# Kernel optimization log

Hardware: AMD Instinct MI355X
Metric: run time of the kernel (lower is better)

## Reference

```python
import jax, jax.numpy as jnp
import numpy as np
from functools import partial

HIDDEN = 512
INTER = 2048
N_EXPERTS = 8
TOP_K = 2
BATCH, SEQ = 2, 2048


def setup_inputs() -> dict:
    key = jax.random.key(0)
    k_x, k_r, k_u, k_d = jax.random.split(key, 4)
    x = jax.random.normal(k_x, (BATCH, SEQ, HIDDEN), dtype=jnp.float32)
    # router: nn.Linear(hidden, n_experts, bias=False); store as (H, E) so logits = x @ w_router
    w_router = jax.random.normal(k_r, (HIDDEN, N_EXPERTS), dtype=jnp.float32) / np.sqrt(HIDDEN)
    # per-expert FFN weights, stored pre-transposed for x @ W
    w_up = jax.random.normal(k_u, (N_EXPERTS, HIDDEN, INTER), dtype=jnp.float32) / np.sqrt(HIDDEN)
    w_down = jax.random.normal(k_d, (N_EXPERTS, INTER, HIDDEN), dtype=jnp.float32) / np.sqrt(INTER)
    return {"x": x, "w_router": w_router, "w_up": w_up, "w_down": w_down}


def _moe_forward(x, w_router, w_up, w_down):
    B, S, H = x.shape
    T = B * S
    xf = x.reshape(T, H)
    logits = xf @ w_router                      # (T, E)
    top_vals, top_idx = jax.lax.top_k(logits, TOP_K)
    rw = jax.nn.softmax(top_vals, axis=-1)      # (T, K) routing weights
    E = w_up.shape[0]
    # combine weight per (token, expert): sum_k rw[t,k] * [sel[t,k]==e]
    cw = jnp.zeros((T, E), dtype=x.dtype).at[
        jnp.arange(T)[:, None], top_idx
    ].add(rw)                                   # (T, E)

    def expert_step(acc, operand):
        wu, wd, we = operand                    # (H,I), (I,H), (T,)
        h = jax.nn.gelu(xf @ wu, approximate=False)  # exact erf GELU (torch nn.GELU default)
        y = h @ wd                              # (T, H)
        return acc + we[:, None] * y, None

    acc0 = jnp.zeros((T, H), dtype=x.dtype)
    acc, _ = jax.lax.scan(expert_step, acc0, (w_up, w_down, cw.T))
    output = acc.reshape(B, S, H)

    # aux load-balance loss
    probs = jax.nn.softmax(logits, axis=-1)
    expert_usage = probs.mean(axis=0)           # (E,)
    load_balance_loss = jnp.sum((expert_usage - 1.0 / E) ** 2)
    return output, load_balance_loss, expert_usage


def reference(x, w_router, w_up, w_down):
    return _moe_forward(x, w_router, w_up, w_down)
```

## Files before the change

kernel.cpp:

```cpp
#include <hip/hip_runtime.h>
#include <hip/hip_bf16.h>
#include <math.h>

#define T_TOKENS 4096
#define HID 512
#define INTER 2048
#define NEXP 8

typedef __bf16 bf16x8 __attribute__((ext_vector_type(8)));
typedef __bf16 bf16x4 __attribute__((ext_vector_type(4)));
typedef float f32x4 __attribute__((ext_vector_type(4)));

#define GLD16(g, l) __builtin_amdgcn_global_load_lds( \
    (const __attribute__((address_space(1))) void*)(g), \
    (__attribute__((address_space(3))) void*)(l), 16, 0, 0)

__device__ __forceinline__ void transpose_tile(const float* __restrict__ in,
                                               __bf16* __restrict__ out,
                                               int R, int C, int r0, int c0,
                                               __bf16 (*tile)[68]) {
  int tid = threadIdx.x;
  int rr = tid >> 4;
  int cc = (tid & 15) * 4;
#pragma unroll
  for (int j = 0; j < 4; ++j) {
    int row = j * 16 + rr;
    float4 v = *(const float4*)(in + (size_t)(r0 + row) * C + c0 + cc);
    tile[row][cc + 0] = (__bf16)v.x;
    tile[row][cc + 1] = (__bf16)v.y;
    tile[row][cc + 2] = (__bf16)v.z;
    tile[row][cc + 3] = (__bf16)v.w;
  }
  __syncthreads();
#pragma unroll
  for (int j = 0; j < 4; ++j) {
    int orow = j * 16 + rr;
    bf16x4 o;
    o[0] = tile[cc + 0][orow];
    o[1] = tile[cc + 1][orow];
    o[2] = tile[cc + 2][orow];
    o[3] = tile[cc + 3][orow];
    *(bf16x4*)(out + (size_t)(c0 + orow) * R + r0 + cc) = o;
  }
}

__global__ void prep_kernel(const float* __restrict__ x, const float* __restrict__ wrt,
                            int* __restrict__ topi, float* __restrict__ topw,
                            int* __restrict__ cntpart, float* __restrict__ usagepart,
                            const float* __restrict__ wu, __bf16* __restrict__ wuT,
                            const float* __restrict__ wd, __bf16* __restrict__ wdT) {
  __shared__ float wsm[8 * 512];
  __shared__ float us[8];
  __shared__ int cs[8];
  __shared__ __bf16 tile[64][68];
  int bid = blockIdx.x;
  int tid = threadIdx.x;

  if (bid >= 3072) {
    int b = bid - 3072;
    int e = b >> 8;
    int c0 = (b & 7) * 64;
    int r0 = ((b >> 3) & 31) * 64;
    transpose_tile(wd + (size_t)e * INTER * HID, wdT + (size_t)e * INTER * HID,
                   INTER, HID, r0, c0, tile);
    return;
  }
  if (bid >= 1024) {
    int b = bid - 1024;
    int e = b >> 8;
    int c0 = (b & 31) * 64;
    int r0 = ((b >> 5) & 7) * 64;
    transpose_tile(wu + (size_t)e * HID * INTER, wuT + (size_t)e * HID * INTER,
                   HID, INTER, r0, c0, tile);
    return;
  }

  if (tid < 8) { us[tid] = 0.f; cs[tid] = 0; }
  for (int i = tid; i < 8 * 512; i += 256) {
    int e = i >> 9, h = i & 511;
    wsm[i] = wrt[h * 8 + e];
  }
  __syncthreads();
  int lane = tid & 63;
  int t = bid * 4 + (tid >> 6);
  const float* xt = x + (size_t)t * HID;
  float a[8];
#pragma unroll
  for (int e = 0; e < 8; ++e) a[e] = 0.f;
#pragma unroll
  for (int j = 0; j < 8; ++j) {
    float xv = xt[lane + j * 64];
#pragma unroll
    for (int e = 0; e < 8; ++e) a[e] += xv * wsm[e * 512 + lane + j * 64];
  }
#pragma unroll
  for (int off = 32; off > 0; off >>= 1) {
#pragma unroll
    for (int e = 0; e < 8; ++e) a[e] += __shfl_xor(a[e], off);
  }
  if (lane == 0) {
    float m = a[0];
#pragma unroll
    for (int e = 1; e < 8; ++e) m = fmaxf(m, a[e]);
    float p[8], s = 0.f;
#pragma unroll
    for (int e = 0; e < 8; ++e) { p[e] = expf(a[e] - m); s += p[e]; }
    float inv = 1.f / s;
#pragma unroll
    for (int e = 0; e < 8; ++e) atomicAdd(&us[e], p[e] * inv);
    int i0 = 0; float v0 = a[0];
#pragma unroll
    for (int e = 1; e < 8; ++e) if (a[e] > v0) { v0 = a[e]; i0 = e; }
    int i1 = -1; float v1 = -3.4e38f;
#pragma unroll
    for (int e = 0; e < 8; ++e) if (e != i0 && a[e] > v1) { v1 = a[e]; i1 = e; }
    float e1 = expf(v1 - v0);
    float w0 = 1.f / (1.f + e1);
    float w1 = e1 * w0;
    topi[t * 2] = i0; topi[t * 2 + 1] = i1;
    topw[t * 2] = w0; topw[t * 2 + 1] = w1;
    atomicAdd(&cs[i0], 1); atomicAdd(&cs[i1], 1);
  }
  __syncthreads();
  if (tid < 8) {
    cntpart[bid * 8 + tid] = cs[tid];
    usagepart[bid * 8 + tid] = us[tid];
  }
}

__global__ void finalize_kernel(const int* __restrict__ cntpart, const float* __restrict__ usagepart,
                                int* __restrict__ cnt, int* __restrict__ off,
                                float* __restrict__ tail) {
  __shared__ int ci[256];
  __shared__ float uf[256];
  int tid = threadIdx.x;
  int e = tid >> 5, c = tid & 31;
  int s = 0; float u = 0.f;
  for (int b = c; b < 1024; b += 32) {
    s += cntpart[b * 8 + e];
    u += usagepart[b * 8 + e];
  }
  ci[tid] = s; uf[tid] = u;
  __syncthreads();
  for (int st = 16; st > 0; st >>= 1) {
    if (c < st) { ci[tid] += ci[tid + st]; uf[tid] += uf[tid + st]; }
    __syncthreads();
  }
  if (tid == 0) {
    int o = 0;
    float loss = 0.f;
    for (int e2 = 0; e2 < 8; ++e2) {
      int ce = ci[e2 * 32];
      cnt[e2] = ce;
      off[e2] = o;
      o += (ce + 127) & ~127;
      float uu = uf[e2 * 32] * (1.0f / 4096.0f);
      tail[1 + e2] = uu;
      float d = uu - 0.125f;
      loss += d * d;
    }
    tail[0] = loss;
  }
}

__global__ void slotassign_kernel(const int* __restrict__ topi, const float* __restrict__ topw,
                                  const int* __restrict__ off, int* __restrict__ cnt2pad,
                                  int* __restrict__ stok, float* __restrict__ sw,
                                  int* __restrict__ slotof) {
  __shared__ int wavehist[16][8];
  __shared__ int blockbase[8];
  int tid = threadIdx.x, lane = tid & 63, wv = tid >> 6;
  int p = blockIdx.x * 1024 + tid;
  int e = topi[p];
  float w = topw[p];
  unsigned long long mymask = 0;
#pragma unroll
  for (int e2 = 0; e2 < 8; ++e2) {
    unsigned long long m = __ballot(e == e2);
    if (lane == 0) wavehist[wv][e2] = __popcll(m);
    if (e2 == e) mymask = m;
  }
  __syncthreads();
  if (tid < 8) {
    int s = 0;
#pragma unroll
    for (int w2 = 0; w2 < 16; ++w2) s += wavehist[w2][tid];
    blockbase[tid] = atomicAdd(&cnt2pad[tid * 16], s);
  }
  __syncthreads();
  int rank = 0;
  for (int w2 = 0; w2 < wv; ++w2) rank += wavehist[w2][e];
  rank += __popcll(mymask & ((1ull << lane) - 1ull));
  int slot = off[e] + blockbase[e] + rank;
  stok[slot] = p >> 1;
  sw[slot] = w;
  slotof[p] = slot;
}

__global__ void gather_kernel(const float* __restrict__ x, const int* __restrict__ slotof,
                              __bf16* __restrict__ Xg) {
  int tid = threadIdx.x, lane = tid & 63;
  int p = blockIdx.x * 4 + (tid >> 6);
  int slot = slotof[p];
  int t = p >> 1;
  const float4* xs = (const float4*)(x + (size_t)t * HID);
  float4 v0 = xs[lane * 2], v1 = xs[lane * 2 + 1];
  bf16x8 o;
  o[0] = (__bf16)v0.x; o[1] = (__bf16)v0.y; o[2] = (__bf16)v0.z; o[3] = (__bf16)v0.w;
  o[4] = (__bf16)v1.x; o[5] = (__bf16)v1.y; o[6] = (__bf16)v1.z; o[7] = (__bf16)v1.w;
  *(bf16x8*)(Xg + (size_t)slot * HID + lane * 8) = o;
}

template <int EPI>
__launch_bounds__(256, 8)
__global__ void gemm64(const __bf16* __restrict__ A, const __bf16* __restrict__ Ball,
                       int lda, int ldb, long sB,
                       __bf16* __restrict__ Hout, int ldh,
                       float* __restrict__ Out,
                       const int* __restrict__ stok, const float* __restrict__ sw,
                       const int* __restrict__ offp, const int* __restrict__ cntp) {
  int bid = blockIdx.x;
  int e = bid & 7;
  int r = bid >> 3;
  int mt, n0, nk;
  if (EPI == 0) {
    n0 = (r & 31) * 64;
    mt = r >> 5;
    nk = 8;
  } else {
    n0 = (r & 7) * 64;
    mt = r >> 3;
    nk = 32;
  }
  int cnte = cntp[e];
  if (mt * 64 >= cnte) return;
  int offe = offp[e];
  int m0 = offe + mt * 64;
  const __bf16* B = Ball + (size_t)e * sB;

  __shared__ char smem[16384];
  char* As = smem;
  char* Bs = smem + 8192;

  int tid = threadIdx.x;
  int lane = tid & 63;
  int wid = tid >> 6;
  int wr = wid >> 1, wc = wid & 1;

  f32x4 acc[2][2];
#pragma unroll
  for (int i = 0; i < 2; ++i)
#pragma unroll
    for (int j = 0; j < 2; ++j) acc[i][j] = (f32x4){0.f, 0.f, 0.f, 0.f};

  for (int it = 0; it < nk; ++it) {
    int k0 = it * 64;
#pragma unroll
    for (int q2 = 0; q2 < 2; ++q2) {
      int L = q2 * 4096 + tid * 16;
      int row = L >> 7;
      int kb = L & 127;
      int kbs = kb ^ ((row & 7) << 4);
      GLD16((const char*)(A + (size_t)(m0 + row) * lda + k0) + kbs, As + L);
      GLD16((const char*)(B + (size_t)(n0 + row) * (size_t)ldb + k0) + kbs, Bs + L);
    }
    __syncthreads();
#pragma unroll
    for (int ks = 0; ks < 2; ++ks) {
      bf16x8 av[2], bv[2];
      int kb = ks * 64 + ((lane >> 4) << 4);
#pragma unroll
      for (int i = 0; i < 2; ++i) {
        int rowA = wr * 32 + i * 16 + (lane & 15);
        av[i] = *(const bf16x8*)(As + rowA * 128 + (kb ^ ((rowA & 7) << 4)));
        int rowB = wc * 32 + i * 16 + (lane & 15);
        bv[i] = *(const bf16x8*)(Bs + rowB * 128 + (kb ^ ((rowB & 7) << 4)));
      }
#pragma unroll
      for (int i = 0; i < 2; ++i)
#pragma unroll
        for (int j = 0; j < 2; ++j)
          acc[i][j] = __builtin_amdgcn_mfma_f32_16x16x32_bf16(av[i], bv[j], acc[i][j], 0, 0, 0);
    }
    __syncthreads();
  }

  int lim = offe + cnte;
  if (EPI == 0) {
#pragma unroll
    for (int i = 0; i < 2; ++i) {
#pragma unroll
      for (int r2 = 0; r2 < 4; ++r2) {
        int slot = m0 + wr * 32 + i * 16 + ((lane >> 4) << 2) + r2;
        if (slot < lim) {
          __bf16* hp = Hout + (size_t)slot * ldh + n0 + wc * 32 + (lane & 15);
#pragma unroll
          for (int j = 0; j < 2; ++j) {
            float v = acc[i][j][r2];
            float g = 0.5f * v * (1.0f + erff(v * 0.70710678118654752f));
            hp[j * 16] = (__bf16)g;
          }
        }
      }
    }
  } else {
#pragma unroll
    for (int i = 0; i < 2; ++i) {
#pragma unroll
      for (int r2 = 0; r2 < 4; ++r2) {
        int slot = m0 + wr * 32 + i * 16 + ((lane >> 4) << 2) + r2;
        if (slot < lim) {
          int t = stok[slot];
          float w = sw[slot];
          float* op = Out + (size_t)t * HID + n0 + wc * 32 + (lane & 15);
#pragma unroll
          for (int j = 0; j < 2; ++j) atomicAdd(op + j * 16, w * acc[i][j][r2]);
        }
      }
    }
  }
}

extern "C" void kernel_launch(void* const* d_in, const int* in_sizes, int n_in,
                              void* d_out, int out_size, void* d_ws, size_t ws_size,
                              hipStream_t stream) {
  const float* x   = (const float*)d_in[0];
  const float* wrt = (const float*)d_in[1];
  const float* wu  = (const float*)d_in[2];
  const float* wd  = (const float*)d_in[3];
  float* out = (float*)d_out;
  char* ws = (char*)d_ws;

  const size_t XG_OFF   = 0;
  const size_t H_OFF    = XG_OFF  + (size_t)9216 * 512 * 2;
  const size_t WUT_OFF  = H_OFF   + (size_t)9216 * 2048 * 2;
  const size_t WDT_OFF  = WUT_OFF + (size_t)8 * 512 * 2048 * 2;
  const size_t TOK_OFF  = WDT_OFF + (size_t)8 * 512 * 2048 * 2;
  const size_t SW_OFF   = TOK_OFF  + (size_t)9216 * 4;
  const size_t TOPI_OFF = SW_OFF   + (size_t)9216 * 4;
  const size_t TOPW_OFF = TOPI_OFF + (size_t)8192 * 4;
  const size_t SLOT_OFF = TOPW_OFF + (size_t)8192 * 4;
  const size_t CPART_OFF = SLOT_OFF + (size_t)8192 * 4;
  const size_t UPART_OFF = CPART_OFF + (size_t)8192 * 4;
  const size_t CTRL_OFF  = UPART_OFF + (size_t)8192 * 4;

  __bf16* Xg   = (__bf16*)(ws + XG_OFF);
  __bf16* H    = (__bf16*)(ws + H_OFF);
  __bf16* wuT  = (__bf16*)(ws + WUT_OFF);
  __bf16* wdT  = (__bf16*)(ws + WDT_OFF);
  int*    stok = (int*)(ws + TOK_OFF);
  float*  sw   = (float*)(ws + SW_OFF);
  int*    topi = (int*)(ws + TOPI_OFF);
  float*  topw = (float*)(ws + TOPW_OFF);
  int*    slotof = (int*)(ws + SLOT_OFF);
  int*    cntpart = (int*)(ws + CPART_OFF);
  float*  usagepart = (float*)(ws + UPART_OFF);
  int*    cnt  = (int*)(ws + CTRL_OFF);
  int*    off  = (int*)(ws + CTRL_OFF + 64);
  int*    cnt2pad = (int*)(ws + CTRL_OFF + 128);

  hipMemsetAsync(ws + CTRL_OFF, 0, 1024, stream);
  hipMemsetAsync(d_out, 0, (size_t)T_TOKENS * HID * 4, stream);

  prep_kernel<<<5120, 256, 0, stream>>>(x, wrt, topi, topw, cntpart, usagepart,
                                        wu, wuT, wd, wdT);
  finalize_kernel<<<1, 256, 0, stream>>>(cntpart, usagepart, cnt, off,
                                         out + (size_t)T_TOKENS * HID);
  slotassign_kernel<<<8, 1024, 0, stream>>>(topi, topw, off, cnt2pad, stok, sw, slotof);
  gather_kernel<<<2048, 256, 0, stream>>>(x, slotof, Xg);

  gemm64<0><<<6144, 256, 0, stream>>>(
      Xg, wuT, HID, HID, (long)INTER * HID, H, INTER,
      nullptr, nullptr, nullptr, off, cnt);
  gemm64<1><<<1536, 256, 0, stream>>>(
      H, wdT, INTER, INTER, (long)INTER * HID, nullptr, 0,
      out, stok, sw, off, cnt);
}
```

Baseline: 123.1 us.

## Fold slot assignment into finalize and gather, drop slotassign kernel and memset

The finalize kernel now computes per-block, per-expert base offsets with a prefix scan over the partial counts. Each gather wave then derives its token's two expert slots locally from topi and those bases, and writes the metadata itself. This removes the separate slotassign launch, its atomics, and a memset. Gather now reads each x row once and writes two bf16 rows, which halves the gather grid. The single-block finalize does slightly more serial work, and slot order becomes deterministic.

```diff
diff --git a/kernel.cpp b/kernel.cpp
--- a/kernel.cpp
+++ b/kernel.cpp
@@ -130,85 +130,87 @@
 
 __global__ void finalize_kernel(const int* __restrict__ cntpart, const float* __restrict__ usagepart,
                                 int* __restrict__ cnt, int* __restrict__ off,
-                                float* __restrict__ tail) {
-  __shared__ int ci[256];
-  __shared__ float uf[256];
+                                int* __restrict__ bbase, float* __restrict__ tail) {
+  __shared__ int cs[8][32];
+  __shared__ float uf[8][32];
+  __shared__ int cpre[8][32];
+  __shared__ int ctot[8];
+  __shared__ int offs[8];
   int tid = threadIdx.x;
   int e = tid >> 5, c = tid & 31;
   int s = 0; float u = 0.f;
-  for (int b = c; b < 1024; b += 32) {
+  for (int b = c * 32; b < c * 32 + 32; ++b) {
     s += cntpart[b * 8 + e];
     u += usagepart[b * 8 + e];
   }
-  ci[tid] = s; uf[tid] = u;
-  __syncthreads();
-  for (int st = 16; st > 0; st >>= 1) {
-    if (c < st) { ci[tid] += ci[tid + st]; uf[tid] += uf[tid + st]; }
-    __syncthreads();
-  }
+  cs[e][c] = s; uf[e][c] = u;
+  __syncthreads();
+  if (c == 0) {
+    int run = 0;
+#pragma unroll
+    for (int cc = 0; cc < 32; ++cc) { cpre[e][cc] = run; run += cs[e][cc]; }
+    ctot[e] = run;
+    cnt[e] = run;
+  }
+  __syncthreads();
   if (tid == 0) {
     int o = 0;
     float loss = 0.f;
     for (int e2 = 0; e2 < 8; ++e2) {
-      int ce = ci[e2 * 32];
-      cnt[e2] = ce;
+      offs[e2] = o;
       off[e2] = o;
-      o += (ce + 127) & ~127;
-      float uu = uf[e2 * 32] * (1.0f / 4096.0f);
+      o += (ctot[e2] + 127) & ~127;
+      float uu = 0.f;
+      for (int cc = 0; cc < 32; ++cc) uu += uf[e2][cc];
+      uu *= (1.0f / 4096.0f);
       tail[1 + e2] = uu;
       float d = uu - 0.125f;
       loss += d * d;
     }
     tail[0] = loss;
   }
-}
-
-__global__ void slotassign_kernel(const int* __restrict__ topi, const float* __restrict__ topw,
-                                  const int* __restrict__ off, int* __restrict__ cnt2pad,
-                                  int* __restrict__ stok, float* __restrict__ sw,
-                                  int* __restrict__ slotof) {
-  __shared__ int wavehist[16][8];
-  __shared__ int blockbase[8];
-  int tid = threadIdx.x, lane = tid & 63, wv = tid >> 6;
-  int p = blockIdx.x * 1024 + tid;
-  int e = topi[p];
-  float w = topw[p];
-  unsigned long long mymask = 0;
-#pragma unroll
-  for (int e2 = 0; e2 < 8; ++e2) {
-    unsigned long long m = __ballot(e == e2);
-    if (lane == 0) wavehist[wv][e2] = __popcll(m);
-    if (e2 == e) mymask = m;
-  }
-  __syncthreads();
-  if (tid < 8) {
-    int s = 0;
-#pragma unroll
-    for (int w2 = 0; w2 < 16; ++w2) s += wavehist[w2][tid];
-    blockbase[tid] = atomicAdd(&cnt2pad[tid * 16], s);
-  }
-  __syncthreads();
-  int rank = 0;
-  for (int w2 = 0; w2 < wv; ++w2) rank += wavehist[w2][e];
-  rank += __popcll(mymask & ((1ull << lane) - 1ull));
-  int slot = off[e] + blockbase[e] + rank;
-  stok[slot] = p >> 1;
-  sw[slot] = w;
-  slotof[p] = slot;
-}
-
-__global__ void gather_kernel(const float* __restrict__ x, const int* __restrict__ slotof,
+  __syncthreads();
+  int base = offs[e] + cpre[e][c];
+  for (int b = c * 32; b < c * 32 + 32; ++b) {
+    bbase[b * 8 + e] = base;
+    base += cntpart[b * 8 + e];
+  }
+}
+
+__global__ void gather_kernel(const float* __restrict__ x, const int* __restrict__ topi,
+                              const float* __restrict__ topw, const int* __restrict__ bbase,
+                              int* __restrict__ stok, float* __restrict__ sw,
                               __bf16* __restrict__ Xg) {
   int tid = threadIdx.x, lane = tid & 63;
-  int p = blockIdx.x * 4 + (tid >> 6);
-  int slot = slotof[p];
-  int t = p >> 1;
+  int t = blockIdx.x * 4 + (tid >> 6);
+  int b = t >> 2;
+  int j = t & 3;
+  int slot0 = 0, slot1 = 0;
+  if (lane == 0) {
+    int ti[8];
+#pragma unroll
+    for (int q = 0; q < 8; ++q) ti[q] = topi[b * 8 + q];
+    int e0 = ti[2 * j], e1 = ti[2 * j + 1];
+    int r0 = 0, r1 = 0;
+#pragma unroll
+    for (int q = 0; q < 8; ++q) {
+      if (q < 2 * j) { r0 += (ti[q] == e0); r1 += (ti[q] == e1); }
+    }
+    r1 += (e0 == e1);
+    slot0 = bbase[b * 8 + e0] + r0;
+    slot1 = bbase[b * 8 + e1] + r1;
+    stok[slot0] = t; sw[slot0] = topw[2 * t];
+    stok[slot1] = t; sw[slot1] = topw[2 * t + 1];
+  }
+  slot0 = __shfl(slot0, 0);
+  slot1 = __shfl(slot1, 0);
   const float4* xs = (const float4*)(x + (size_t)t * HID);
   float4 v0 = xs[lane * 2], v1 = xs[lane * 2 + 1];
   bf16x8 o;
   o[0] = (__bf16)v0.x; o[1] = (__bf16)v0.y; o[2] = (__bf16)v0.z; o[3] = (__bf16)v0.w;
   o[4] = (__bf16)v1.x; o[5] = (__bf16)v1.y; o[6] = (__bf16)v1.z; o[7] = (__bf16)v1.w;
-  *(bf16x8*)(Xg + (size_t)slot * HID + lane * 8) = o;
+  *(bf16x8*)(Xg + (size_t)slot0 * HID + lane * 8) = o;
+  *(bf16x8*)(Xg + (size_t)slot1 * HID + lane * 8) = o;
 }
 
 template <int EPI>
@@ -339,8 +341,8 @@
   const size_t SW_OFF   = TOK_OFF  + (size_t)9216 * 4;
   const size_t TOPI_OFF = SW_OFF   + (size_t)9216 * 4;
   const size_t TOPW_OFF = TOPI_OFF + (size_t)8192 * 4;
-  const size_t SLOT_OFF = TOPW_OFF + (size_t)8192 * 4;
-  const size_t CPART_OFF = SLOT_OFF + (size_t)8192 * 4;
+  const size_t BBASE_OFF = TOPW_OFF + (size_t)8192 * 4;
+  const size_t CPART_OFF = BBASE_OFF + (size_t)8192 * 4;
   const size_t UPART_OFF = CPART_OFF + (size_t)8192 * 4;
   const size_t CTRL_OFF  = UPART_OFF + (size_t)8192 * 4;
 
@@ -352,22 +354,19 @@
   float*  sw   = (float*)(ws + SW_OFF);
   int*    topi = (int*)(ws + TOPI_OFF);
   float*  topw = (float*)(ws + TOPW_OFF);
-  int*    slotof = (int*)(ws + SLOT_OFF);
+  int*    bbase = (int*)(ws + BBASE_OFF);
   int*    cntpart = (int*)(ws + CPART_OFF);
   float*  usagepart = (float*)(ws + UPART_OFF);
   int*    cnt  = (int*)(ws + CTRL_OFF);
   int*    off  = (int*)(ws + CTRL_OFF + 64);
-  int*    cnt2pad = (int*)(ws + CTRL_OFF + 128);
-
-  hipMemsetAsync(ws + CTRL_OFF, 0, 1024, stream);
+
   hipMemsetAsync(d_out, 0, (size_t)T_TOKENS * HID * 4, stream);
 
   prep_kernel<<<5120, 256, 0, stream>>>(x, wrt, topi, topw, cntpart, usagepart,
                                         wu, wuT, wd, wdT);
-  finalize_kernel<<<1, 256, 0, stream>>>(cntpart, usagepart, cnt, off,
+  finalize_kernel<<<1, 256, 0, stream>>>(cntpart, usagepart, cnt, off, bbase,
                                          out + (size_t)T_TOKENS * HID);
-  slotassign_kernel<<<8, 1024, 0, stream>>>(topi, topw, off, cnt2pad, stok, sw, slotof);
-  gather_kernel<<<2048, 256, 0, stream>>>(x, slotof, Xg);
+  gather_kernel<<<1024, 256, 0, stream>>>(x, topi, topw, bbase, stok, sw, Xg);
 
   gemm64<0><<<6144, 256, 0, stream>>>(
       Xg, wuT, HID, HID, (long)INTER * HID, H, INTER,
```

Measured after the change: 124.0 us. About the same (+0.7%).
